# Performance work log

Measured on AMD Instinct MI355X. Metric: run time of the kernel, lower is better.

Reference implementation:

```python
import jax, jax.numpy as jnp
import numpy as np

N_FACTS = 512
D = 256          # object_dim == query_dim
HG = 256         # g hidden / output width
HF1, HF2 = 256, 512
OUT_F = 159


def setup_inputs() -> dict:
    key = jax.random.key(0)
    ks = jax.random.split(key, 16)
    s = 0.02
    return {
        "x": jax.random.normal(ks[0], (N_FACTS, D), dtype=jnp.float32),
        "q": jax.random.normal(ks[1], (D,), dtype=jnp.float32),
        # MLP g: input 3*D -> 256 -> 256 -> 256, ReLU after every layer (nonlinear=True)
        "g_W1": jax.random.normal(ks[2], (3 * D, HG), dtype=jnp.float32) * s,
        "g_b1": jnp.zeros((HG,), dtype=jnp.float32),
        "g_W2": jax.random.normal(ks[3], (HG, HG), dtype=jnp.float32) * s,
        "g_b2": jnp.zeros((HG,), dtype=jnp.float32),
        "g_W3": jax.random.normal(ks[4], (HG, HG), dtype=jnp.float32) * s,
        "g_b3": jnp.zeros((HG,), dtype=jnp.float32),
        # MLP f: 256 -> 256 -> 512 -> 159, ReLU on hidden layers only
        "f_W1": jax.random.normal(ks[5], (HG, HF1), dtype=jnp.float32) * s,
        "f_b1": jnp.zeros((HF1,), dtype=jnp.float32),
        "f_W2": jax.random.normal(ks[6], (HF1, HF2), dtype=jnp.float32) * s,
        "f_b2": jnp.zeros((HF2,), dtype=jnp.float32),
        "f_W3": jax.random.normal(ks[7], (HF2, OUT_F), dtype=jnp.float32) * s,
        "f_b3": jnp.zeros((OUT_F,), dtype=jnp.float32),
    }


def reference(x, q, g_W1, g_b1, g_W2, g_b2, g_W3, g_b3,
              f_W1, f_b1, f_W2, f_b2, f_W3, f_b3):
    # Original builds pair_concat[k] = cat(x[i], x[j], q) for k = j*n + i.
    # Decompose g's first linear over the concat blocks to avoid materializing
    # the (n^2, 3D) tensor: same math, three small matmuls + broadcast add.
    d = x.shape[1]
    a = x @ g_W1[:d]            # (n, HG), contribution of xi
    b = x @ g_W1[d:2 * d]       # (n, HG), contribution of xj
    c = q @ g_W1[2 * d:]        # (HG,),  contribution of q
    # pair (j, i): xj varies along axis 0, xi along axis 1
    h = jax.nn.relu(b[:, None, :] + a[None, :, :] + c + g_b1)   # (n, n, HG)
    h = jax.nn.relu(h @ g_W2 + g_b2)
    rel = jax.nn.relu(h @ g_W3 + g_b3)                          # (n, n, HG)
    emb = rel.sum(axis=(0, 1))[None, :]                         # (1, HG) = sum over all pairs
    y = jax.nn.relu(emb @ f_W1 + f_b1)
    y = jax.nn.relu(y @ f_W2 + f_b2)
    out = y @ f_W3 + f_b3                                       # (1, OUT_F)
    return out
```

## Files before the change

kernel.cpp:

```cpp
#include <hip/hip_runtime.h>
#include <hip/hip_bf16.h>

#define NF 512
#define HG 256

typedef __attribute__((ext_vector_type(4))) float  f32x4;
typedef __attribute__((ext_vector_type(8))) __bf16 bf16x8;
typedef __attribute__((ext_vector_type(8))) short  s16x8;

static __device__ __forceinline__ unsigned short f2bf(float x) {
    unsigned int u = __float_as_uint(x);
    u = (u + 0x7fffu + ((u >> 16) & 1u)) >> 16;
    return (unsigned short)u;
}

__global__ __launch_bounds__(256) void prep_ab(
    const float* __restrict__ x, const float* __restrict__ q,
    const float* __restrict__ gW1, const float* __restrict__ gb1,
    float* __restrict__ a, float* __restrict__ b,
    float* __restrict__ cc, float* __restrict__ emb)
{
    const int t = threadIdx.x;
    const int bid = blockIdx.x;
    if (bid == 128) {
        float acc = gb1[t];
        #pragma unroll 8
        for (int d = 0; d < 256; ++d) acc = fmaf(q[d], gW1[(512 + d) * 256 + t], acc);
        cc[t] = acc;
        emb[t] = 0.f;
        return;
    }
    __shared__ float xs[4][256];
    const int r0 = bid * 4;
    #pragma unroll
    for (int r = 0; r < 4; ++r) xs[r][t] = x[(r0 + r) * 256 + t];
    __syncthreads();
    float aa[4] = {0.f, 0.f, 0.f, 0.f}, bb[4] = {0.f, 0.f, 0.f, 0.f};
    #pragma unroll 4
    for (int d = 0; d < 256; ++d) {
        const float wa = gW1[d * 256 + t];
        const float wb = gW1[(256 + d) * 256 + t];
        #pragma unroll
        for (int r = 0; r < 4; ++r) {
            aa[r] = fmaf(xs[r][d], wa, aa[r]);
            bb[r] = fmaf(xs[r][d], wb, bb[r]);
        }
    }
    #pragma unroll
    for (int r = 0; r < 4; ++r) {
        a[(r0 + r) * 256 + t] = aa[r];
        b[(r0 + r) * 256 + t] = bb[r];
    }
}

__global__ __launch_bounds__(256) void prep_wt(
    const float* __restrict__ gW2, const float* __restrict__ gW3,
    unsigned short* __restrict__ w2t, unsigned short* __restrict__ w3t)
{
    __shared__ unsigned short tile[64][65];
    const int bid = blockIdx.x;
    const float* src = (bid < 16) ? gW2 : gW3;
    unsigned short* dst = (bid < 16) ? w2t : w3t;
    const int b = bid & 15;
    const int br = (b >> 2) * 64;
    const int bc = (b & 3) * 64;
    const int t = threadIdx.x;
    const int tr = t >> 6;
    const int tc = t & 63;
    #pragma unroll
    for (int rr = 0; rr < 16; ++rr) {
        const int r = tr * 16 + rr;
        tile[r][tc] = f2bf(src[(br + r) * 256 + bc + tc]);
    }
    __syncthreads();
    #pragma unroll
    for (int rr = 0; rr < 16; ++rr) {
        const int r = tr * 16 + rr;
        dst[(bc + r) * 256 + br + tc] = tile[tc][r];
    }
}

__global__ __launch_bounds__(512, 2) void rn_main(
    const float* __restrict__ ga, const float* __restrict__ gb,
    const float* __restrict__ cc,
    const unsigned short* __restrict__ w2t, const unsigned short* __restrict__ w3t,
    const float* __restrict__ gb2, const float* __restrict__ gb3,
    float* __restrict__ emb)
{
    __shared__ float bc_s[256];
    __shared__ unsigned short h1[32 * 256];
    __shared__ unsigned short h2[32 * 256];

    const int t = threadIdx.x;
    const int j = blockIdx.x;
    const int lane = t & 63;
    const int wave = t >> 6;
    const int l16 = lane & 15;
    const int lk = lane >> 4;
    const int wcol = wave * 32;

    if (t < 256) bc_s[t] = gb[j * 256 + t] + cc[t];

    bf16x8 B2[2][8], B3[2][8];
    float bias2[2], bias3[2];
    #pragma unroll
    for (int ns = 0; ns < 2; ++ns) {
        const int col = wcol + ns * 16 + l16;
        bias2[ns] = gb2[col];
        bias3[ns] = gb3[col];
        #pragma unroll
        for (int ks = 0; ks < 8; ++ks) {
            const int koff = ks * 32 + lk * 8;
            B2[ns][ks] = *reinterpret_cast<const bf16x8*>(w2t + col * 256 + koff);
            B3[ns][ks] = *reinterpret_cast<const bf16x8*>(w3t + col * 256 + koff);
        }
    }
    float colsum[2] = {0.f, 0.f};
    __syncthreads();

    for (int it = 0; it < 16; ++it) {
        const int i0 = it * 32;
        #pragma unroll
        for (int r = 0; r < 2; ++r) {
            const int idx = t + r * 512;
            const int m = idx >> 5;
            const int k0 = (idx & 31) << 3;
            const f32x4 a0 = *reinterpret_cast<const f32x4*>(ga + (i0 + m) * 256 + k0);
            const f32x4 a1 = *reinterpret_cast<const f32x4*>(ga + (i0 + m) * 256 + k0 + 4);
            const f32x4 c0 = *reinterpret_cast<const f32x4*>(bc_s + k0);
            const f32x4 c1 = *reinterpret_cast<const f32x4*>(bc_s + k0 + 4);
            s16x8 pk;
            #pragma unroll
            for (int e = 0; e < 4; ++e) {
                float v0 = a0[e] + c0[e]; v0 = v0 > 0.f ? v0 : 0.f;
                float v1 = a1[e] + c1[e]; v1 = v1 > 0.f ? v1 : 0.f;
                pk[e]     = (short)f2bf(v0);
                pk[e + 4] = (short)f2bf(v1);
            }
            *reinterpret_cast<s16x8*>(&h1[(m * 256 + k0) ^ ((m & 7) << 3)]) = pk;
        }
        __syncthreads();

        #pragma unroll
        for (int ms = 0; ms < 2; ++ms) {
            const int row = ms * 16 + l16;
            bf16x8 A[8];
            #pragma unroll
            for (int ks = 0; ks < 8; ++ks) {
                const int koff = ks * 32 + lk * 8;
                A[ks] = *reinterpret_cast<const bf16x8*>(&h1[(row * 256 + koff) ^ ((row & 7) << 3)]);
            }
            #pragma unroll
            for (int ns = 0; ns < 2; ++ns) {
                f32x4 acc = {0.f, 0.f, 0.f, 0.f};
                #pragma unroll
                for (int ks = 0; ks < 8; ++ks)
                    acc = __builtin_amdgcn_mfma_f32_16x16x32_bf16(A[ks], B2[ns][ks], acc, 0, 0, 0);
                const int ccol = wcol + ns * 16 + l16;
                #pragma unroll
                for (int reg = 0; reg < 4; ++reg) {
                    float v = acc[reg] + bias2[ns];
                    v = v > 0.f ? v : 0.f;
                    const int rr = ms * 16 + lk * 4 + reg;
                    h2[(rr * 256 + ccol) ^ ((rr & 7) << 3)] = f2bf(v);
                }
            }
        }
        __syncthreads();

        #pragma unroll
        for (int ms = 0; ms < 2; ++ms) {
            const int row = ms * 16 + l16;
            bf16x8 A[8];
            #pragma unroll
            for (int ks = 0; ks < 8; ++ks) {
                const int koff = ks * 32 + lk * 8;
                A[ks] = *reinterpret_cast<const bf16x8*>(&h2[(row * 256 + koff) ^ ((row & 7) << 3)]);
            }
            #pragma unroll
            for (int ns = 0; ns < 2; ++ns) {
                f32x4 acc = {0.f, 0.f, 0.f, 0.f};
                #pragma unroll
                for (int ks = 0; ks < 8; ++ks)
                    acc = __builtin_amdgcn_mfma_f32_16x16x32_bf16(A[ks], B3[ns][ks], acc, 0, 0, 0);
                float s = 0.f;
                #pragma unroll
                for (int reg = 0; reg < 4; ++reg) {
                    float v = acc[reg] + bias3[ns];
                    s += (v > 0.f ? v : 0.f);
                }
                colsum[ns] += s;
            }
        }
    }

    #pragma unroll
    for (int ns = 0; ns < 2; ++ns) {
        float v = colsum[ns];
        v += __shfl_xor(v, 16, 64);
        v += __shfl_xor(v, 32, 64);
        if (lane < 16) atomicAdd(&emb[wcol + ns * 16 + l16], v);
    }
}

__global__ __launch_bounds__(512) void rn_final(
    const float* __restrict__ emb,
    const float* __restrict__ fW1, const float* __restrict__ fb1,
    const float* __restrict__ fW2, const float* __restrict__ fb2,
    const float* __restrict__ fW3, const float* __restrict__ fb3,
    float* __restrict__ out)
{
    __shared__ float e_s[256], y1_s[256], y2_s[512];
    const int t = threadIdx.x;
    if (t < 256) e_s[t] = emb[t];
    __syncthreads();
    if (t < 256) {
        float acc = fb1[t];
        #pragma unroll 8
        for (int k = 0; k < 256; ++k) acc = fmaf(e_s[k], fW1[k * 256 + t], acc);
        y1_s[t] = acc > 0.f ? acc : 0.f;
    }
    __syncthreads();
    {
        float acc = fb2[t];
        #pragma unroll 8
        for (int k = 0; k < 256; ++k) acc = fmaf(y1_s[k], fW2[k * 512 + t], acc);
        y2_s[t] = acc > 0.f ? acc : 0.f;
    }
    __syncthreads();
    if (t < 159) {
        float acc = fb3[t];
        #pragma unroll 8
        for (int k = 0; k < 512; ++k) acc = fmaf(y2_s[k], fW3[k * 159 + t], acc);
        out[t] = acc;
    }
}

extern "C" void kernel_launch(void* const* d_in, const int* in_sizes, int n_in,
                              void* d_out, int out_size, void* d_ws, size_t ws_size,
                              hipStream_t stream)
{
    const float* x   = (const float*)d_in[0];
    const float* q   = (const float*)d_in[1];
    const float* gW1 = (const float*)d_in[2];
    const float* gb1 = (const float*)d_in[3];
    const float* gW2 = (const float*)d_in[4];
    const float* gb2 = (const float*)d_in[5];
    const float* gW3 = (const float*)d_in[6];
    const float* gb3 = (const float*)d_in[7];
    const float* fW1 = (const float*)d_in[8];
    const float* fb1 = (const float*)d_in[9];
    const float* fW2 = (const float*)d_in[10];
    const float* fb2 = (const float*)d_in[11];
    const float* fW3 = (const float*)d_in[12];
    const float* fb3 = (const float*)d_in[13];
    float* out = (float*)d_out;

    char* ws = (char*)d_ws;
    float* a_  = (float*)(ws);
    float* b_  = (float*)(ws + 512 * 1024);
    float* cc  = (float*)(ws + 1024 * 1024);
    float* emb = (float*)(ws + 1024 * 1024 + 1024);
    unsigned short* w2t = (unsigned short*)(ws + 1024 * 1024 + 2048);
    unsigned short* w3t = (unsigned short*)(ws + 1024 * 1024 + 2048 + 128 * 1024);

    prep_ab<<<129, 256, 0, stream>>>(x, q, gW1, gb1, a_, b_, cc, emb);
    prep_wt<<<32, 256, 0, stream>>>(gW2, gW3, w2t, w3t);
    rn_main<<<512, 512, 0, stream>>>(a_, b_, cc, w2t, w3t, gb2, gb3, emb);
    rn_final<<<1, 512, 0, stream>>>(emb, fW1, fb1, fW2, fb2, fW3, fb3, out);
}
```

Baseline: 235.0 us.

## Fuse prep kernels, double tile rows, overlap h1 generation, split-K final MLP

Merges the two prep kernels into one launch and processes 64 rows per iteration in the main kernel, halving the loop trip count. The next tile's first-layer activations are now generated between the two MFMA stages, overlapping global loads with compute. The final MLP splits its K dimension across 1024 threads with a shared-memory reduction. bf16 conversion now uses native casts. Doubling the LDS buffers to 64KB may limit occupancy at 2 blocks per CU.

After: 219.2 us. 6.7% less time.

```diff
diff --git a/kernel.cpp b/kernel.cpp
--- a/kernel.cpp
+++ b/kernel.cpp
@@ -1,82 +1,72 @@
 #include <hip/hip_runtime.h>
 #include <hip/hip_bf16.h>
 
-#define NF 512
-#define HG 256
-
 typedef __attribute__((ext_vector_type(4))) float  f32x4;
 typedef __attribute__((ext_vector_type(8))) __bf16 bf16x8;
-typedef __attribute__((ext_vector_type(8))) short  s16x8;
-
-static __device__ __forceinline__ unsigned short f2bf(float x) {
-    unsigned int u = __float_as_uint(x);
-    u = (u + 0x7fffu + ((u >> 16) & 1u)) >> 16;
-    return (unsigned short)u;
-}
-
-__global__ __launch_bounds__(256) void prep_ab(
+
+static __device__ __forceinline__ unsigned short bfbits(float x) {
+    return __builtin_bit_cast(unsigned short, (__bf16)x);
+}
+
+__global__ __launch_bounds__(256) void prep_all(
     const float* __restrict__ x, const float* __restrict__ q,
     const float* __restrict__ gW1, const float* __restrict__ gb1,
+    const float* __restrict__ gW2, const float* __restrict__ gW3,
     float* __restrict__ a, float* __restrict__ b,
-    float* __restrict__ cc, float* __restrict__ emb)
+    float* __restrict__ cc, float* __restrict__ emb,
+    unsigned short* __restrict__ w2t, unsigned short* __restrict__ w3t)
 {
     const int t = threadIdx.x;
     const int bid = blockIdx.x;
-    if (bid == 128) {
+    if (bid < 128) {
+        __shared__ float xs[4][256];
+        const int r0 = bid * 4;
+        #pragma unroll
+        for (int r = 0; r < 4; ++r) xs[r][t] = x[(r0 + r) * 256 + t];
+        __syncthreads();
+        float aa[4] = {0.f, 0.f, 0.f, 0.f}, bb[4] = {0.f, 0.f, 0.f, 0.f};
+        #pragma unroll 4
+        for (int d = 0; d < 256; ++d) {
+            const float wa = gW1[d * 256 + t];
+            const float wb = gW1[(256 + d) * 256 + t];
+            #pragma unroll
+            for (int r = 0; r < 4; ++r) {
+                aa[r] = fmaf(xs[r][d], wa, aa[r]);
+                bb[r] = fmaf(xs[r][d], wb, bb[r]);
+            }
+        }
+        #pragma unroll
+        for (int r = 0; r < 4; ++r) {
+            a[(r0 + r) * 256 + t] = aa[r];
+            b[(r0 + r) * 256 + t] = bb[r];
+        }
+    } else if (bid == 128) {
         float acc = gb1[t];
         #pragma unroll 8
         for (int d = 0; d < 256; ++d) acc = fmaf(q[d], gW1[(512 + d) * 256 + t], acc);
         cc[t] = acc;
         emb[t] = 0.f;
-        return;
-    }
-    __shared__ float xs[4][256];
-    const int r0 = bid * 4;
-    #pragma unroll
-    for (int r = 0; r < 4; ++r) xs[r][t] = x[(r0 + r) * 256 + t];
-    __syncthreads();
-    float aa[4] = {0.f, 0.f, 0.f, 0.f}, bb[4] = {0.f, 0.f, 0.f, 0.f};
-    #pragma unroll 4
-    for (int d = 0; d < 256; ++d) {
-        const float wa = gW1[d * 256 + t];
-        const float wb = gW1[(256 + d) * 256 + t];
-        #pragma unroll
-        for (int r = 0; r < 4; ++r) {
-            aa[r] = fmaf(xs[r][d], wa, aa[r]);
-            bb[r] = fmaf(xs[r][d], wb, bb[r]);
-        }
-    }
-    #pragma unroll
-    for (int r = 0; r < 4; ++r) {
-        a[(r0 + r) * 256 + t] = aa[r];
-        b[(r0 + r) * 256 + t] = bb[r];
-    }
-}
-
-__global__ __launch_bounds__(256) void prep_wt(
-    const float* __restrict__ gW2, const float* __restrict__ gW3,
-    unsigned short* __restrict__ w2t, unsigned short* __restrict__ w3t)
-{
-    __shared__ unsigned short tile[64][65];
-    const int bid = blockIdx.x;
-    const float* src = (bid < 16) ? gW2 : gW3;
-    unsigned short* dst = (bid < 16) ? w2t : w3t;
-    const int b = bid & 15;
-    const int br = (b >> 2) * 64;
-    const int bc = (b & 3) * 64;
-    const int t = threadIdx.x;
-    const int tr = t >> 6;
-    const int tc = t & 63;
-    #pragma unroll
-    for (int rr = 0; rr < 16; ++rr) {
-        const int r = tr * 16 + rr;
-        tile[r][tc] = f2bf(src[(br + r) * 256 + bc + tc]);
-    }
-    __syncthreads();
-    #pragma unroll
-    for (int rr = 0; rr < 16; ++rr) {
-        const int r = tr * 16 + rr;
-        dst[(bc + r) * 256 + br + tc] = tile[tc][r];
+    } else {
+        __shared__ unsigned short tile[64][65];
+        const int bb_ = bid - 129;
+        const float* src = (bb_ < 16) ? gW2 : gW3;
+        unsigned short* dst = (bb_ < 16) ? w2t : w3t;
+        const int bidx = bb_ & 15;
+        const int br = (bidx >> 2) * 64;
+        const int bc = (bidx & 3) * 64;
+        const int tr = t >> 6;
+        const int tc = t & 63;
+        #pragma unroll
+        for (int rr = 0; rr < 16; ++rr) {
+            const int r = tr * 16 + rr;
+            tile[r][tc] = bfbits(src[(br + r) * 256 + bc + tc]);
+        }
+        __syncthreads();
+        #pragma unroll
+        for (int rr = 0; rr < 16; ++rr) {
+            const int r = tr * 16 + rr;
+            dst[(bc + r) * 256 + br + tc] = tile[tc][r];
+        }
     }
 }
 
@@ -87,9 +77,8 @@
     const float* __restrict__ gb2, const float* __restrict__ gb3,
     float* __restrict__ emb)
 {
-    __shared__ float bc_s[256];
-    __shared__ unsigned short h1[32 * 256];
-    __shared__ unsigned short h2[32 * 256];
+    __shared__ __bf16 h1[64 * 256];
+    __shared__ __bf16 h2[64 * 256];
 
     const int t = threadIdx.x;
     const int j = blockIdx.x;
@@ -99,7 +88,16 @@
     const int lk = lane >> 4;
     const int wcol = wave * 32;
 
-    if (t < 256) bc_s[t] = gb[j * 256 + t] + cc[t];
+    const int k0 = (t & 31) << 3;
+    f32x4 bc0, bc1;
+    {
+        const f32x4 g0 = *reinterpret_cast<const f32x4*>(gb + j * 256 + k0);
+        const f32x4 g1 = *reinterpret_cast<const f32x4*>(gb + j * 256 + k0 + 4);
+        const f32x4 c0 = *reinterpret_cast<const f32x4*>(cc + k0);
+        const f32x4 c1 = *reinterpret_cast<const f32x4*>(cc + k0 + 4);
+        #pragma unroll
+        for (int e = 0; e < 4; ++e) { bc0[e] = g0[e] + c0[e]; bc1[e] = g1[e] + c1[e]; }
+    }
 
     bf16x8 B2[2][8], B3[2][8];
     float bias2[2], bias3[2];
@@ -116,33 +114,30 @@
         }
     }
     float colsum[2] = {0.f, 0.f};
-    __syncthreads();
-
-    for (int it = 0; it < 16; ++it) {
-        const int i0 = it * 32;
-        #pragma unroll
-        for (int r = 0; r < 2; ++r) {
-            const int idx = t + r * 512;
-            const int m = idx >> 5;
-            const int k0 = (idx & 31) << 3;
-            const f32x4 a0 = *reinterpret_cast<const f32x4*>(ga + (i0 + m) * 256 + k0);
-            const f32x4 a1 = *reinterpret_cast<const f32x4*>(ga + (i0 + m) * 256 + k0 + 4);
-            const f32x4 c0 = *reinterpret_cast<const f32x4*>(bc_s + k0);
-            const f32x4 c1 = *reinterpret_cast<const f32x4*>(bc_s + k0 + 4);
-            s16x8 pk;
-            #pragma unroll
-            for (int e = 0; e < 4; ++e) {
-                float v0 = a0[e] + c0[e]; v0 = v0 > 0.f ? v0 : 0.f;
-                float v1 = a1[e] + c1[e]; v1 = v1 > 0.f ? v1 : 0.f;
-                pk[e]     = (short)f2bf(v0);
-                pk[e + 4] = (short)f2bf(v1);
-            }
-            *reinterpret_cast<s16x8*>(&h1[(m * 256 + k0) ^ ((m & 7) << 3)]) = pk;
-        }
-        __syncthreads();
-
-        #pragma unroll
-        for (int ms = 0; ms < 2; ++ms) {
+
+    #define GEN_H1(I0)                                                              \
+    {                                                                               \
+        _Pragma("unroll")                                                           \
+        for (int r = 0; r < 4; ++r) {                                               \
+            const int m = (t >> 5) + r * 16;                                        \
+            const f32x4 a0 = *reinterpret_cast<const f32x4*>(ga + ((I0) + m) * 256 + k0);     \
+            const f32x4 a1 = *reinterpret_cast<const f32x4*>(ga + ((I0) + m) * 256 + k0 + 4); \
+            bf16x8 pk;                                                              \
+            _Pragma("unroll")                                                       \
+            for (int e = 0; e < 4; ++e) {                                           \
+                pk[e]     = (__bf16)fmaxf(a0[e] + bc0[e], 0.f);                     \
+                pk[e + 4] = (__bf16)fmaxf(a1[e] + bc1[e], 0.f);                     \
+            }                                                                       \
+            *reinterpret_cast<bf16x8*>(&h1[(m * 256 + k0) ^ ((m & 7) << 3)]) = pk;  \
+        }                                                                           \
+    }
+
+    GEN_H1(0);
+    __syncthreads();
+
+    for (int it = 0; it < 8; ++it) {
+        #pragma unroll
+        for (int ms = 0; ms < 4; ++ms) {
             const int row = ms * 16 + l16;
             bf16x8 A[8];
             #pragma unroll
@@ -159,17 +154,17 @@
                 const int ccol = wcol + ns * 16 + l16;
                 #pragma unroll
                 for (int reg = 0; reg < 4; ++reg) {
-                    float v = acc[reg] + bias2[ns];
-                    v = v > 0.f ? v : 0.f;
+                    const float v = fmaxf(acc[reg] + bias2[ns], 0.f);
                     const int rr = ms * 16 + lk * 4 + reg;
-                    h2[(rr * 256 + ccol) ^ ((rr & 7) << 3)] = f2bf(v);
+                    h2[(rr * 256 + ccol) ^ ((rr & 7) << 3)] = (__bf16)v;
                 }
             }
         }
         __syncthreads();
 
-        #pragma unroll
-        for (int ms = 0; ms < 2; ++ms) {
+        if (it < 7) GEN_H1((it + 1) * 64);
+        #pragma unroll
+        for (int ms = 0; ms < 4; ++ms) {
             const int row = ms * 16 + l16;
             bf16x8 A[8];
             #pragma unroll
@@ -185,13 +180,12 @@
                     acc = __builtin_amdgcn_mfma_f32_16x16x32_bf16(A[ks], B3[ns][ks], acc, 0, 0, 0);
                 float s = 0.f;
                 #pragma unroll
-                for (int reg = 0; reg < 4; ++reg) {
-                    float v = acc[reg] + bias3[ns];
-                    s += (v > 0.f ? v : 0.f);
-                }
+                for (int reg = 0; reg < 4; ++reg)
+                    s += fmaxf(acc[reg] + bias3[ns], 0.f);
                 colsum[ns] += s;
             }
         }
+        __syncthreads();
     }
 
     #pragma unroll
@@ -201,39 +195,56 @@
         v += __shfl_xor(v, 32, 64);
         if (lane < 16) atomicAdd(&emb[wcol + ns * 16 + l16], v);
     }
-}
-
-__global__ __launch_bounds__(512) void rn_final(
+    #undef GEN_H1
+}
+
+__global__ __launch_bounds__(1024) void rn_final(
     const float* __restrict__ emb,
     const float* __restrict__ fW1, const float* __restrict__ fb1,
     const float* __restrict__ fW2, const float* __restrict__ fb2,
     const float* __restrict__ fW3, const float* __restrict__ fb3,
     float* __restrict__ out)
 {
-    __shared__ float e_s[256], y1_s[256], y2_s[512];
+    __shared__ float e_s[256];
+    __shared__ float red[1024];
+    __shared__ float y1[256];
+    __shared__ float y2[512];
     const int t = threadIdx.x;
     if (t < 256) e_s[t] = emb[t];
     __syncthreads();
-    if (t < 256) {
-        float acc = fb1[t];
+    {
+        const int col = t & 255, ks = t >> 8;
+        float acc = 0.f;
         #pragma unroll 8
-        for (int k = 0; k < 256; ++k) acc = fmaf(e_s[k], fW1[k * 256 + t], acc);
-        y1_s[t] = acc > 0.f ? acc : 0.f;
-    }
-    __syncthreads();
-    {
-        float acc = fb2[t];
+        for (int k = ks * 64; k < ks * 64 + 64; ++k) acc = fmaf(e_s[k], fW1[k * 256 + col], acc);
+        red[ks * 256 + col] = acc;
+    }
+    __syncthreads();
+    if (t < 256)
+        y1[t] = fmaxf(red[t] + red[256 + t] + red[512 + t] + red[768 + t] + fb1[t], 0.f);
+    __syncthreads();
+    {
+        const int col = t & 511, ks = t >> 9;
+        float acc = 0.f;
         #pragma unroll 8
-        for (int k = 0; k < 256; ++k) acc = fmaf(y1_s[k], fW2[k * 512 + t], acc);
-        y2_s[t] = acc > 0.f ? acc : 0.f;
-    }
-    __syncthreads();
-    if (t < 159) {
-        float acc = fb3[t];
-        #pragma unroll 8
-        for (int k = 0; k < 512; ++k) acc = fmaf(y2_s[k], fW3[k * 159 + t], acc);
-        out[t] = acc;
-    }
+        for (int k = ks * 128; k < ks * 128 + 128; ++k) acc = fmaf(y1[k], fW2[k * 512 + col], acc);
+        red[ks * 512 + col] = acc;
+    }
+    __syncthreads();
+    if (t < 512) y2[t] = fmaxf(red[t] + red[512 + t] + fb2[t], 0.f);
+    __syncthreads();
+    {
+        const int col = t & 255, ks = t >> 8;
+        if (col < 159) {
+            float acc = 0.f;
+            #pragma unroll 8
+            for (int k = ks * 128; k < ks * 128 + 128; ++k) acc = fmaf(y2[k], fW3[k * 159 + col], acc);
+            red[ks * 256 + col] = acc;
+        }
+    }
+    __syncthreads();
+    if (t < 159)
+        out[t] = red[t] + red[256 + t] + red[512 + t] + red[768 + t] + fb3[t];
 }
 
 extern "C" void kernel_launch(void* const* d_in, const int* in_sizes, int n_in,
@@ -264,8 +275,7 @@
     unsigned short* w2t = (unsigned short*)(ws + 1024 * 1024 + 2048);
     unsigned short* w3t = (unsigned short*)(ws + 1024 * 1024 + 2048 + 128 * 1024);
 
-    prep_ab<<<129, 256, 0, stream>>>(x, q, gW1, gb1, a_, b_, cc, emb);
-    prep_wt<<<32, 256, 0, stream>>>(gW2, gW3, w2t, w3t);
+    prep_all<<<161, 256, 0, stream>>>(x, q, gW1, gb1, gW2, gW3, a_, b_, cc, emb, w2t, w3t);
     rn_main<<<512, 512, 0, stream>>>(a_, b_, cc, w2t, w3t, gb2, gb3, emb);
-    rn_final<<<1, 512, 0, stream>>>(emb, fW1, fb1, fW2, fb2, fW3, fb3, out);
-}
+    rn_final<<<1, 1024, 0, stream>>>(emb, fW1, fb1, fW2, fb2, fW3, fb3, out);
+}
```
